# Kernel tuning notes

Hardware: AMD Instinct MI355X
Metric: run time of the kernel (lower is better)

## Reference

```python
import jax, jax.numpy as jnp
import numpy as np

GROUPS = 32
EPS = 1e-6


def _group_norm(x, scale, bias):
    B, C, H, W = x.shape
    xg = x.reshape(B, GROUPS, C // GROUPS, H, W)
    mean = xg.mean(axis=(2, 3, 4), keepdims=True)
    var = xg.var(axis=(2, 3, 4), keepdims=True)
    xg = (xg - mean) * jax.lax.rsqrt(var + EPS)
    x = xg.reshape(B, C, H, W)
    return x * scale[None, :, None, None] + bias[None, :, None, None]


def setup_inputs() -> dict:
    key = jax.random.key(0)
    ks = jax.random.split(key, 8)
    B, C, H, W = 4, 256, 64, 64
    s = 1.0 / np.sqrt(C)
    return {
        "x": jax.random.normal(ks[0], (B, C, H, W), jnp.float32),
        "gn_scale": jnp.ones((C,), jnp.float32),
        "gn_bias": jnp.zeros((C,), jnp.float32),
        "wq": jax.random.normal(ks[1], (C, C), jnp.float32) * s,
        "bq": jnp.zeros((C,), jnp.float32),
        "wk": jax.random.normal(ks[2], (C, C), jnp.float32) * s,
        "bk": jnp.zeros((C,), jnp.float32),
        "wv": jax.random.normal(ks[3], (C, C), jnp.float32) * s,
        "bv": jnp.zeros((C,), jnp.float32),
        "wp": jax.random.normal(ks[4], (C, C), jnp.float32) * s,
        "bp": jnp.zeros((C,), jnp.float32),
    }


def reference(x, gn_scale, gn_bias, wq, bq, wk, bk, wv, bv, wp, bp):
    B, C, H, W = x.shape
    hw = H * W
    o = _group_norm(x, gn_scale, gn_bias)           # [B,C,H,W]
    of = o.reshape(B, C, hw)                         # [B,C,hw]
    # 1x1 convs == per-pixel channel matmuls
    q = jnp.einsum('oc,bcn->bno', wq, of) + bq[None, None, :]   # [B,hw,C]
    k = jnp.einsum('oc,bcn->bon', wk, of) + bk[None, :, None]   # [B,C,hw]
    v = jnp.einsum('oc,bcn->bon', wv, of) + bv[None, :, None]   # [B,C,hw]
    w = jnp.einsum('bic,bcj->bij', q, k) * (C ** -0.5)          # [B,hw,hw]
    w = jax.nn.softmax(w, axis=2)
    # o[b,c,i] = sum_j v[b,c,j] * w[b,i,j]
    attn = jnp.einsum('bcj,bij->bci', v, w)          # [B,C,hw]
    # faithful to original: reshape to (B,C,W,H) (requires H==W)
    attn = attn.reshape(B, C, W, H)
    out = jnp.einsum('oc,bchw->bohw', wp, attn) + bp[None, :, None, None]
    return out + x
```

## Files before the change

### kernel.cpp

```cpp
#include <hip/hip_runtime.h>
#include <hip/hip_bf16.h>

#define NB 4
#define NC 256
#define NHW 4096
#define CPG 8
#define GEPS 1e-6f

typedef __hip_bfloat16 bf16;
typedef __attribute__((ext_vector_type(8))) short bf16x8;
typedef __attribute__((ext_vector_type(4))) float f32x4;
typedef __attribute__((ext_vector_type(8))) unsigned short u16x8;

#define MFMA16(A,B,C) __builtin_amdgcn_mfma_f32_16x16x32_bf16(A,B,C,0,0,0)

typedef __attribute__((address_space(1))) const unsigned int as1_uint;
typedef __attribute__((address_space(3))) unsigned int as3_uint;
__device__ __forceinline__ void gload_lds16(const void* g, void* l){
  __builtin_amdgcn_global_load_lds((as1_uint*)g, (as3_uint*)l, 16, 0, 0);
}

__device__ __forceinline__ float u2f(unsigned short u){
  union { unsigned u32; float f; } w; w.u32 = ((unsigned)u) << 16; return w.f;
}
__device__ __forceinline__ bf16 f2b(float v){ return __float2bfloat16(v); }
__device__ __forceinline__ unsigned short f2bu(float v){
  union { bf16 h; unsigned short u; } w; w.h = __float2bfloat16(v); return w.u;
}

__global__ __launch_bounds__(256)
void gn_stats_kernel(const float* __restrict__ x, float* __restrict__ stats){
  const int bg = blockIdx.x;
  const float* p = x + (size_t)bg * (CPG * NHW);
  float s = 0.f, s2 = 0.f;
  for(int i = threadIdx.x * 4; i < CPG * NHW; i += 1024){
    float4 v = *(const float4*)(p + i);
    s  += v.x + v.y + v.z + v.w;
    s2 += v.x*v.x + v.y*v.y + v.z*v.z + v.w*v.w;
  }
  __shared__ float red[256];
  red[threadIdx.x] = s; __syncthreads();
  for(int t = 128; t > 0; t >>= 1){
    if(threadIdx.x < t) red[threadIdx.x] += red[threadIdx.x + t];
    __syncthreads();
  }
  float sum = red[0]; __syncthreads();
  red[threadIdx.x] = s2; __syncthreads();
  for(int t = 128; t > 0; t >>= 1){
    if(threadIdx.x < t) red[threadIdx.x] += red[threadIdx.x + t];
    __syncthreads();
  }
  if(threadIdx.x == 0){
    const float inv_n = 1.f / (float)(CPG * NHW);
    float mean = sum * inv_n;
    float var = red[0] * inv_n - mean * mean;
    if(var < 0.f) var = 0.f;
    stats[bg * 2]     = mean;
    stats[bg * 2 + 1] = rsqrtf(var + GEPS);
  }
}

__global__ __launch_bounds__(256)
void wprep_kernel(const float* __restrict__ wq, const float* __restrict__ wk,
                  const float* __restrict__ wv, const float* __restrict__ wp,
                  const float* __restrict__ bq, const float* __restrict__ bk,
                  const float* __restrict__ bv,
                  bf16* __restrict__ wqkv, bf16* __restrict__ wpb, float* __restrict__ bqs){
  int i = blockIdx.x * 256 + threadIdx.x;
  if(i < 196608){
    float v;
    if(i < 65536)       v = wq[i] * 0.0625f;
    else if(i < 131072) v = wk[i - 65536];
    else                v = wv[i - 131072];
    wqkv[i] = f2b(v);
  } else {
    int j = i - 196608;
    wpb[j] = f2b(wp[j]);
  }
  if(i < 768) bqs[i] = (i < 256) ? bq[i] * 0.0625f : (i < 512 ? bk[i - 256] : bv[i - 512]);
}

__global__ __launch_bounds__(256)
void gn_prep_kernel(const float* __restrict__ x, const float* __restrict__ stats,
                    const float* __restrict__ gsc, const float* __restrict__ gbi,
                    bf16* __restrict__ xt){
  const int b = blockIdx.z, cB = blockIdx.y * 64, nB = blockIdx.x * 64;
  __shared__ unsigned short Tt[64][80];
  const int tid = threadIdx.x;
  const float* xb = x + ((size_t)(b * NC + cB)) * NHW + nB;
  #pragma unroll
  for(int pass = 0; pass < 4; pass++){
    int c_loc = (tid >> 4) + pass * 16;
    int n0 = (tid & 15) * 4;
    float4 v = *(const float4*)(xb + (size_t)c_loc * NHW + n0);
    int c_abs = cB + c_loc, bg = b * 32 + (c_abs >> 3);
    float a = stats[bg * 2 + 1] * gsc[c_abs];
    float d = gbi[c_abs] - stats[bg * 2] * a;
    Tt[n0 + 0][c_loc] = f2bu(v.x * a + d);
    Tt[n0 + 1][c_loc] = f2bu(v.y * a + d);
    Tt[n0 + 2][c_loc] = f2bu(v.z * a + d);
    Tt[n0 + 3][c_loc] = f2bu(v.w * a + d);
  }
  __syncthreads();
  int n_loc = tid >> 2, cq = (tid & 3) * 16;
  u16x8 w0 = *(const u16x8*)&Tt[n_loc][cq];
  u16x8 w1 = *(const u16x8*)&Tt[n_loc][cq + 8];
  unsigned short* dst = (unsigned short*)xt + ((size_t)(b * NHW + nB + n_loc)) * NC + cB + cq;
  *(u16x8*)dst = w0;
  *(u16x8*)(dst + 8) = w1;
}

__global__ __launch_bounds__(256, 2)
void gemm_kernel(const bf16* __restrict__ Wb, const bf16* __restrict__ Bm,
                 const float* __restrict__ bias,
                 bf16* __restrict__ qo, bf16* __restrict__ ko, bf16* __restrict__ vo,
                 float* __restrict__ fo, const float* __restrict__ xres, int epi){
  const int nB = blockIdx.x * 128;
  const int oB = blockIdx.y * 128;
  const int tid = threadIdx.x;
  const int wave = tid >> 6, lane = tid & 63;
  const int l15 = lane & 15, quad = lane >> 4;
  const int wx = wave & 1, wy = wave >> 1;

  __shared__ __align__(16) unsigned short Ast[2][512 * 8];
  __shared__ __align__(16) unsigned short Bst[2][512 * 8];
  __shared__ __align__(16) unsigned short Tt[128 * 136];

  const short* Wp = (const short*)Wb;
  const short* Bp = (const short*)Bm;

  f32x4 acc[4][4];
  #pragma unroll
  for(int mi = 0; mi < 4; mi++)
    #pragma unroll
    for(int ni = 0; ni < 4; ni++) acc[mi][ni] = (f32x4){0.f, 0.f, 0.f, 0.f};

  #pragma unroll
  for(int t = 0; t < 2; t++){
    int qn0 = (wave * 2 + t) * 64, qn = qn0 + lane;
    int o = qn >> 2, slot = qn & 3;
    gload_lds16(Wp + (size_t)(oB + o) * NC + ((slot ^ (o & 3)) * 8), &Ast[0][qn0 * 8]);
  }
  #pragma unroll
  for(int t = 0; t < 2; t++){
    int qn0 = (wave * 2 + t) * 64, qn = qn0 + lane;
    int n = qn >> 2, slot = qn & 3;
    gload_lds16(Bp + (size_t)(nB + n) * NC + ((slot ^ (n & 3)) * 8), &Bst[0][qn0 * 8]);
  }

  for(int kt = 0; kt < 8; kt++){
    __syncthreads();
    const int p = kt & 1;
    if(kt < 7){
      const int k0 = (kt + 1) * 32;
      #pragma unroll
      for(int t = 0; t < 2; t++){
        int qn0 = (wave * 2 + t) * 64, qn = qn0 + lane;
        int o = qn >> 2, slot = qn & 3;
        gload_lds16(Wp + (size_t)(oB + o) * NC + k0 + ((slot ^ (o & 3)) * 8), &Ast[p ^ 1][qn0 * 8]);
      }
      #pragma unroll
      for(int t = 0; t < 2; t++){
        int qn0 = (wave * 2 + t) * 64, qn = qn0 + lane;
        int n = qn >> 2, slot = qn & 3;
        gload_lds16(Bp + (size_t)(nB + n) * NC + k0 + ((slot ^ (n & 3)) * 8), &Bst[p ^ 1][qn0 * 8]);
      }
    }
    bf16x8 Af[4], Bf[4];
    #pragma unroll
    for(int mi = 0; mi < 4; mi++){
      int o = wx * 64 + mi * 16 + l15;
      Af[mi] = *(const bf16x8*)&Ast[p][(o * 4 + (quad ^ (o & 3))) * 8];
    }
    #pragma unroll
    for(int ni = 0; ni < 4; ni++){
      int n = wy * 64 + ni * 16 + l15;
      Bf[ni] = *(const bf16x8*)&Bst[p][(n * 4 + (quad ^ (n & 3))) * 8];
    }
    #pragma unroll
    for(int mi = 0; mi < 4; mi++)
      #pragma unroll
      for(int ni = 0; ni < 4; ni++)
        acc[mi][ni] = MFMA16(Af[mi], Bf[ni], acc[mi][ni]);
  }

  float bi[4][4];
  #pragma unroll
  for(int mi = 0; mi < 4; mi++)
    #pragma unroll
    for(int r = 0; r < 4; r++)
      bi[mi][r] = bias[oB + wx * 64 + mi * 16 + quad * 4 + r];

  if(epi == 1){
    #pragma unroll
    for(int mi = 0; mi < 4; mi++){
      #pragma unroll
      for(int ni = 0; ni < 4; ni++){
        int na = nB + wy * 64 + ni * 16 + l15;
        #pragma unroll
        for(int r = 0; r < 4; r++){
          int c = oB + wx * 64 + mi * 16 + quad * 4 + r;
          size_t idx = ((size_t)(na >> 12) * NC + c) * NHW + (na & 4095);
          fo[idx] = acc[mi][ni][r] + bi[mi][r] + xres[idx];
        }
      }
    }
  } else if(oB >= 512){
    #pragma unroll
    for(int mi = 0; mi < 4; mi++){
      #pragma unroll
      for(int ni = 0; ni < 4; ni++){
        int na = nB + wy * 64 + ni * 16 + l15;
        #pragma unroll
        for(int r = 0; r < 4; r++){
          int c = oB - 512 + wx * 64 + mi * 16 + quad * 4 + r;
          vo[((size_t)(na >> 12) * NC + c) * NHW + (na & 4095)] = f2b(acc[mi][ni][r] + bi[mi][r]);
        }
      }
    }
  } else {
    #pragma unroll
    for(int mi = 0; mi < 4; mi++){
      int ob = wx * 64 + mi * 16 + quad * 4;
      #pragma unroll
      for(int ni = 0; ni < 4; ni++){
        int nl = wy * 64 + ni * 16 + l15;
        ushort4 pk;
        pk.x = f2bu(acc[mi][ni][0] + bi[mi][0]);
        pk.y = f2bu(acc[mi][ni][1] + bi[mi][1]);
        pk.z = f2bu(acc[mi][ni][2] + bi[mi][2]);
        pk.w = f2bu(acc[mi][ni][3] + bi[mi][3]);
        *(ushort4*)&Tt[nl * 136 + ob] = pk;
      }
    }
    __syncthreads();
    bf16* dst = (oB < 256) ? qo : ko;
    const int oc0 = oB & 255;
    int row = tid >> 1, half = tid & 1;
    unsigned short* gp = (unsigned short*)dst + (size_t)(nB + row) * NC + oc0 + half * 64;
    #pragma unroll
    for(int j = 0; j < 8; j++){
      u16x8 w = *(const u16x8*)&Tt[row * 136 + half * 64 + j * 8];
      *(u16x8*)(gp + j * 8) = w;
    }
  }
}

__global__ __launch_bounds__(256, 2)
void flash_mfma4_kernel(const bf16* __restrict__ qg, const bf16* __restrict__ ktg,
                        const bf16* __restrict__ vg, bf16* __restrict__ Opart,
                        float* __restrict__ lpart){
  const int b = blockIdx.y, h = blockIdx.z;
  const int i0 = blockIdx.x * 128;
  const int tid = threadIdx.x;
  const int wave = tid >> 6, lane = tid & 63;
  const int l15 = lane & 15, quad = lane >> 4;

  __shared__ __align__(16) unsigned short Kt[2][1024 * 8];
  __shared__ __align__(16) unsigned short Vt[2][1024 * 8];
  __shared__ __align__(16) unsigned short Pt_all[4][32 * 40];
  unsigned short* Pt = Pt_all[wave];

  bf16x8 Qf[2][8];
  #pragma unroll
  for(int ist = 0; ist < 2; ist++){
    const short* qp = (const short*)qg +
        ((size_t)b * NHW + i0 + wave * 32 + ist * 16 + l15) * NC + quad * 8;
    #pragma unroll
    for(int ks = 0; ks < 8; ks++) Qf[ist][ks] = *(const bf16x8*)(qp + ks * 32);
  }

  const short* kb = (const short*)ktg + ((size_t)b * NHW + h * 1024) * NC;
  const short* vb = (const short*)vg + (size_t)b * NC * NHW + h * 1024;

  f32x4 O[2][16];
  #pragma unroll
  for(int ist = 0; ist < 2; ist++)
    #pragma unroll
    for(int ct = 0; ct < 16; ct++) O[ist][ct] = (f32x4){0.f, 0.f, 0.f, 0.f};
  float lr0 = 0.f, lr1 = 0.f;

  #pragma unroll
  for(int t = 0; t < 4; t++){
    int qn0 = (wave * 4 + t) * 64, qn = qn0 + lane;
    int j = qn >> 5, slot = qn & 31;
    gload_lds16(kb + (size_t)j * NC + ((slot ^ (j & 7)) * 8), &Kt[0][qn0 * 8]);
  }
  #pragma unroll
  for(int t = 0; t < 4; t++){
    int qn0 = (wave * 4 + t) * 64, qn = qn0 + lane;
    int c = qn >> 2, slot = qn & 3;
    gload_lds16(vb + (size_t)c * NHW + ((slot ^ (c & 3)) * 8), &Vt[0][qn0 * 8]);
  }

  for(int jt = 0; jt < 32; jt++){
    __syncthreads();
    const int p = jt & 1;
    if(jt < 31){
      const int j0n = (jt + 1) * 32;
      #pragma unroll
      for(int t = 0; t < 4; t++){
        int qn0 = (wave * 4 + t) * 64, qn = qn0 + lane;
        int j = qn >> 5, slot = qn & 31;
        gload_lds16(kb + (size_t)(j0n + j) * NC + ((slot ^ (j & 7)) * 8), &Kt[p ^ 1][qn0 * 8]);
      }
      #pragma unroll
      for(int t = 0; t < 4; t++){
        int qn0 = (wave * 4 + t) * 64, qn = qn0 + lane;
        int c = qn >> 2, slot = qn & 3;
        gload_lds16(vb + (size_t)c * NHW + j0n + ((slot ^ (c & 3)) * 8), &Vt[p ^ 1][qn0 * 8]);
      }
    }
    f32x4 S[2][2];
    #pragma unroll
    for(int st = 0; st < 2; st++){
      S[st][0] = (f32x4){0.f, 0.f, 0.f, 0.f};
      S[st][1] = (f32x4){0.f, 0.f, 0.f, 0.f};
      const int j = st * 16 + l15;
      const unsigned short* kr = &Kt[p][(size_t)j * 256];
      #pragma unroll
      for(int ks = 0; ks < 8; ks++){
        int slot = (ks * 4 + quad) ^ (j & 7);
        bf16x8 kf = *(const bf16x8*)&kr[slot * 8];
        S[st][0] = MFMA16(kf, Qf[0][ks], S[st][0]);
        S[st][1] = MFMA16(kf, Qf[1][ks], S[st][1]);
      }
    }
    #pragma unroll
    for(int ist = 0; ist < 2; ist++){
      #pragma unroll
      for(int st = 0; st < 2; st++){
        f32x4 sv = S[st][ist];
        float p0 = __expf(sv[0]), p1 = __expf(sv[1]);
        float p2 = __expf(sv[2]), p3 = __expf(sv[3]);
        if(ist == 0) lr0 += (p0 + p1) + (p2 + p3);
        else         lr1 += (p0 + p1) + (p2 + p3);
        ushort4 pk; pk.x = f2bu(p0); pk.y = f2bu(p1); pk.z = f2bu(p2); pk.w = f2bu(p3);
        *(ushort4*)&Pt[(ist * 16 + l15) * 40 + st * 16 + quad * 4] = pk;
      }
    }
    bf16x8 Pf0 = *(const bf16x8*)&Pt[(l15) * 40 + quad * 8];
    bf16x8 Pf1 = *(const bf16x8*)&Pt[(16 + l15) * 40 + quad * 8];
    #pragma unroll
    for(int ct = 0; ct < 16; ct++){
      int c = ct * 16 + l15;
      bf16x8 vf = *(const bf16x8*)&Vt[p][(c * 4 + (quad ^ (c & 3))) * 8];
      O[0][ct] = MFMA16(Pf0, vf, O[0][ct]);
      O[1][ct] = MFMA16(Pf1, vf, O[1][ct]);
    }
  }

  lr0 += __shfl_xor(lr0, 16); lr0 += __shfl_xor(lr0, 32);
  lr1 += __shfl_xor(lr1, 16); lr1 += __shfl_xor(lr1, 32);

  const size_t hb = (size_t)(h * NB + b) * NHW;
  #pragma unroll
  for(int ist = 0; ist < 2; ist++){
    #pragma unroll
    for(int r = 0; r < 4; r++){
      int i = i0 + wave * 32 + ist * 16 + quad * 4 + r;
      unsigned short* od = (unsigned short*)Opart + (hb + i) * NC + l15;
      #pragma unroll
      for(int ct = 0; ct < 16; ct++) od[ct * 16] = f2bu(O[ist][ct][r]);
    }
  }
  if(lane < 16){
    lpart[hb + i0 + wave * 32 + l15]      = lr0;
    lpart[hb + i0 + wave * 32 + 16 + l15] = lr1;
  }
}

__global__ __launch_bounds__(256)
void flash_combine4_kernel(const bf16* __restrict__ Opart, const float* __restrict__ lpart,
                           bf16* __restrict__ attn){
  int t = blockIdx.x * 256 + threadIdx.x;
  int ng = t >> 3;
  int c0 = (t & 7) * 32;
  const int HS = NB * NHW;
  float l = lpart[ng] + lpart[HS + ng] + lpart[2 * HS + ng] + lpart[3 * HS + ng];
  float inv = 1.f / l;
  const unsigned short* O0 = (const unsigned short*)Opart + (size_t)ng * NC + c0;
  unsigned short* dst = (unsigned short*)attn + (size_t)ng * NC + c0;
  #pragma unroll
  for(int u = 0; u < 32; u += 8){
    u16x8 a0 = *(const u16x8*)(O0 + u);
    u16x8 a1 = *(const u16x8*)(O0 + (size_t)HS * NC + u);
    u16x8 a2 = *(const u16x8*)(O0 + (size_t)2 * HS * NC + u);
    u16x8 a3 = *(const u16x8*)(O0 + (size_t)3 * HS * NC + u);
    u16x8 o;
    #pragma unroll
    for(int e = 0; e < 8; e++)
      o[e] = f2bu((u2f(a0[e]) + u2f(a1[e]) + u2f(a2[e]) + u2f(a3[e])) * inv);
    *(u16x8*)(dst + u) = o;
  }
}

extern "C" void kernel_launch(void* const* d_in, const int* in_sizes, int n_in,
                              void* d_out, int out_size, void* d_ws, size_t ws_size,
                              hipStream_t stream){
  (void)in_sizes; (void)n_in; (void)out_size; (void)ws_size;
  const float* x        = (const float*)d_in[0];
  const float* gn_scale = (const float*)d_in[1];
  const float* gn_bias  = (const float*)d_in[2];
  const float* wq = (const float*)d_in[3];  const float* bq = (const float*)d_in[4];
  const float* wk = (const float*)d_in[5];  const float* bk = (const float*)d_in[6];
  const float* wv = (const float*)d_in[7];  const float* bv = (const float*)d_in[8];
  const float* wp = (const float*)d_in[9];  const float* bp = (const float*)d_in[10];
  float* out = (float*)d_out;

  char* ws = (char*)d_ws;
  const size_t MB = 1048576;
  float* stats = (float*)ws;
  float* bqs   = (float*)(ws + 4096);
  bf16* wqkv   = (bf16*)(ws + 8192);
  bf16* wpb    = (bf16*)(ws + 8192 + 393216);
  bf16* xt     = (bf16*)(ws + 1 * MB);
  bf16* Opart  = xt;
  bf16* q      = (bf16*)(ws + 33 * MB);
  bf16* k      = (bf16*)(ws + 41 * MB);
  bf16* v      = (bf16*)(ws + 49 * MB);
  float* lpart = (float*)(ws + 57 * MB);
  bf16* attn   = q;

  gn_stats_kernel<<<128, 256, 0, stream>>>(x, stats);
  wprep_kernel<<<1024, 256, 0, stream>>>(wq, wk, wv, wp, bq, bk, bv, wqkv, wpb, bqs);
  gn_prep_kernel<<<dim3(64, 4, NB), 256, 0, stream>>>(x, stats, gn_scale, gn_bias, xt);

  gemm_kernel<<<dim3(128, 6), 256, 0, stream>>>(
      wqkv, xt, bqs, q, k, v, nullptr, nullptr, 0);

  flash_mfma4_kernel<<<dim3(32, NB, 4), 256, 0, stream>>>(q, k, v, Opart, lpart);
  flash_combine4_kernel<<<512, 256, 0, stream>>>(Opart, lpart, attn);

  gemm_kernel<<<dim3(128, 2), 256, 0, stream>>>(
      wpb, attn, bp, nullptr, nullptr, nullptr, out, x, 1);
}
```

Measured before the change: 224.1 us.

## Read K straight from global in flash kernel, stage output through LDS, merge prep kernels

Measured after the change: 322.3 us. 43.8% more time.

```diff
diff --git a/kernel.cpp b/kernel.cpp
--- a/kernel.cpp
+++ b/kernel.cpp
@@ -29,7 +29,27 @@
 }
 
 __global__ __launch_bounds__(256)
-void gn_stats_kernel(const float* __restrict__ x, float* __restrict__ stats){
+void gn_stats_wprep_kernel(const float* __restrict__ x, float* __restrict__ stats,
+                           const float* __restrict__ wq, const float* __restrict__ wk,
+                           const float* __restrict__ wv, const float* __restrict__ wp,
+                           const float* __restrict__ bq, const float* __restrict__ bk,
+                           const float* __restrict__ bv,
+                           bf16* __restrict__ wqkv, bf16* __restrict__ wpb,
+                           float* __restrict__ bqs){
+  if(blockIdx.x >= 128){
+    int i = (blockIdx.x - 128) * 256 + threadIdx.x;
+    if(i < 196608){
+      float v;
+      if(i < 65536)       v = wq[i] * 0.0625f;
+      else if(i < 131072) v = wk[i - 65536];
+      else                v = wv[i - 131072];
+      wqkv[i] = f2b(v);
+    } else {
+      wpb[i - 196608] = f2b(wp[i - 196608]);
+    }
+    if(i < 768) bqs[i] = (i < 256) ? bq[i] * 0.0625f : (i < 512 ? bk[i - 256] : bv[i - 512]);
+    return;
+  }
   const int bg = blockIdx.x;
   const float* p = x + (size_t)bg * (CPG * NHW);
   float s = 0.f, s2 = 0.f;
@@ -58,26 +78,6 @@
     stats[bg * 2]     = mean;
     stats[bg * 2 + 1] = rsqrtf(var + GEPS);
   }
-}
-
-__global__ __launch_bounds__(256)
-void wprep_kernel(const float* __restrict__ wq, const float* __restrict__ wk,
-                  const float* __restrict__ wv, const float* __restrict__ wp,
-                  const float* __restrict__ bq, const float* __restrict__ bk,
-                  const float* __restrict__ bv,
-                  bf16* __restrict__ wqkv, bf16* __restrict__ wpb, float* __restrict__ bqs){
-  int i = blockIdx.x * 256 + threadIdx.x;
-  if(i < 196608){
-    float v;
-    if(i < 65536)       v = wq[i] * 0.0625f;
-    else if(i < 131072) v = wk[i - 65536];
-    else                v = wv[i - 131072];
-    wqkv[i] = f2b(v);
-  } else {
-    int j = i - 196608;
-    wpb[j] = f2b(wp[j]);
-  }
-  if(i < 768) bqs[i] = (i < 256) ? bq[i] * 0.0625f : (i < 512 ? bk[i - 256] : bv[i - 512]);
 }
 
 __global__ __launch_bounds__(256)
@@ -247,7 +247,7 @@
 }
 
 __global__ __launch_bounds__(256, 2)
-void flash_mfma4_kernel(const bf16* __restrict__ qg, const bf16* __restrict__ ktg,
+void flash_mfma5_kernel(const bf16* __restrict__ qg, const bf16* __restrict__ ktg,
                         const bf16* __restrict__ vg, bf16* __restrict__ Opart,
                         float* __restrict__ lpart){
   const int b = blockIdx.y, h = blockIdx.z;
@@ -256,7 +256,6 @@
   const int wave = tid >> 6, lane = tid & 63;
   const int l15 = lane & 15, quad = lane >> 4;
 
-  __shared__ __align__(16) unsigned short Kt[2][1024 * 8];
   __shared__ __align__(16) unsigned short Vt[2][1024 * 8];
   __shared__ __align__(16) unsigned short Pt_all[4][32 * 40];
   unsigned short* Pt = Pt_all[wave];
@@ -283,14 +282,8 @@
   #pragma unroll
   for(int t = 0; t < 4; t++){
     int qn0 = (wave * 4 + t) * 64, qn = qn0 + lane;
-    int j = qn >> 5, slot = qn & 31;
-    gload_lds16(kb + (size_t)j * NC + ((slot ^ (j & 7)) * 8), &Kt[0][qn0 * 8]);
-  }
-  #pragma unroll
-  for(int t = 0; t < 4; t++){
-    int qn0 = (wave * 4 + t) * 64, qn = qn0 + lane;
-    int c = qn >> 2, slot = qn & 3;
-    gload_lds16(vb + (size_t)c * NHW + ((slot ^ (c & 3)) * 8), &Vt[0][qn0 * 8]);
+    int c = qn >> 2, slot = qn & 3, gc = slot ^ ((c >> 1) & 3);
+    gload_lds16(vb + (size_t)c * NHW + gc * 8, &Vt[0][qn0 * 8]);
   }
 
   for(int jt = 0; jt < 32; jt++){
@@ -301,27 +294,20 @@
       #pragma unroll
       for(int t = 0; t < 4; t++){
         int qn0 = (wave * 4 + t) * 64, qn = qn0 + lane;
-        int j = qn >> 5, slot = qn & 31;
-        gload_lds16(kb + (size_t)(j0n + j) * NC + ((slot ^ (j & 7)) * 8), &Kt[p ^ 1][qn0 * 8]);
-      }
-      #pragma unroll
-      for(int t = 0; t < 4; t++){
-        int qn0 = (wave * 4 + t) * 64, qn = qn0 + lane;
-        int c = qn >> 2, slot = qn & 3;
-        gload_lds16(vb + (size_t)c * NHW + j0n + ((slot ^ (c & 3)) * 8), &Vt[p ^ 1][qn0 * 8]);
-      }
-    }
+        int c = qn >> 2, slot = qn & 3, gc = slot ^ ((c >> 1) & 3);
+        gload_lds16(vb + (size_t)c * NHW + j0n + gc * 8, &Vt[p ^ 1][qn0 * 8]);
+      }
+    }
+    const int j0 = jt * 32;
     f32x4 S[2][2];
     #pragma unroll
     for(int st = 0; st < 2; st++){
       S[st][0] = (f32x4){0.f, 0.f, 0.f, 0.f};
       S[st][1] = (f32x4){0.f, 0.f, 0.f, 0.f};
-      const int j = st * 16 + l15;
-      const unsigned short* kr = &Kt[p][(size_t)j * 256];
+      const short* kp = kb + (size_t)(j0 + st * 16 + l15) * NC + quad * 8;
       #pragma unroll
       for(int ks = 0; ks < 8; ks++){
-        int slot = (ks * 4 + quad) ^ (j & 7);
-        bf16x8 kf = *(const bf16x8*)&kr[slot * 8];
+        bf16x8 kf = *(const bf16x8*)(kp + ks * 32);
         S[st][0] = MFMA16(kf, Qf[0][ks], S[st][0]);
         S[st][1] = MFMA16(kf, Qf[1][ks], S[st][1]);
       }
@@ -344,7 +330,8 @@
     #pragma unroll
     for(int ct = 0; ct < 16; ct++){
       int c = ct * 16 + l15;
-      bf16x8 vf = *(const bf16x8*)&Vt[p][(c * 4 + (quad ^ (c & 3))) * 8];
+      int slot = quad ^ ((c >> 1) & 3);
+      bf16x8 vf = *(const bf16x8*)&Vt[p][(c * 4 + slot) * 8];
       O[0][ct] = MFMA16(Pf0, vf, O[0][ct]);
       O[1][ct] = MFMA16(Pf1, vf, O[1][ct]);
     }
@@ -353,20 +340,28 @@
   lr0 += __shfl_xor(lr0, 16); lr0 += __shfl_xor(lr0, 32);
   lr1 += __shfl_xor(lr1, 16); lr1 += __shfl_xor(lr1, 32);
 
+  __syncthreads();
+  unsigned short* Vs = &Vt[0][0] + wave * 4096;
   const size_t hb = (size_t)(h * NB + b) * NHW;
   #pragma unroll
   for(int ist = 0; ist < 2; ist++){
     #pragma unroll
-    for(int r = 0; r < 4; r++){
-      int i = i0 + wave * 32 + ist * 16 + quad * 4 + r;
-      unsigned short* od = (unsigned short*)Opart + (hb + i) * NC + l15;
-      #pragma unroll
-      for(int ct = 0; ct < 16; ct++) od[ct * 16] = f2bu(O[ist][ct][r]);
-    }
-  }
-  if(lane < 16){
-    lpart[hb + i0 + wave * 32 + l15]      = lr0;
-    lpart[hb + i0 + wave * 32 + 16 + l15] = lr1;
+    for(int r = 0; r < 4; r++)
+      #pragma unroll
+      for(int ct = 0; ct < 16; ct++)
+        Vs[(quad * 4 + r) * 256 + ct * 16 + l15] = f2bu(O[ist][ct][r]);
+    int row = lane >> 2, c0 = (lane & 3) * 64;
+    unsigned short* gp = (unsigned short*)Opart +
+        (hb + i0 + wave * 32 + ist * 16 + row) * NC + c0;
+    #pragma unroll
+    for(int t = 0; t < 8; t++){
+      u16x8 w = *(const u16x8*)&Vs[row * 256 + c0 + t * 8];
+      *(u16x8*)(gp + t * 8) = w;
+    }
+  }
+  if(lane < 32){
+    float lv = (lane < 16) ? lr0 : lr1;
+    lpart[hb + i0 + wave * 32 + lane] = lv;
   }
 }
 
@@ -422,14 +417,14 @@
   float* lpart = (float*)(ws + 57 * MB);
   bf16* attn   = q;
 
-  gn_stats_kernel<<<128, 256, 0, stream>>>(x, stats);
-  wprep_kernel<<<1024, 256, 0, stream>>>(wq, wk, wv, wp, bq, bk, bv, wqkv, wpb, bqs);
+  gn_stats_wprep_kernel<<<1152, 256, 0, stream>>>(
+      x, stats, wq, wk, wv, wp, bq, bk, bv, wqkv, wpb, bqs);
   gn_prep_kernel<<<dim3(64, 4, NB), 256, 0, stream>>>(x, stats, gn_scale, gn_bias, xt);
 
   gemm_kernel<<<dim3(128, 6), 256, 0, stream>>>(
       wqkv, xt, bqs, q, k, v, nullptr, nullptr, 0);
 
-  flash_mfma4_kernel<<<dim3(32, NB, 4), 256, 0, stream>>>(q, k, v, Opart, lpart);
+  flash_mfma5_kernel<<<dim3(32, NB, 4), 256, 0, stream>>>(q, k, v, Opart, lpart);
   flash_combine4_kernel<<<512, 256, 0, stream>>>(Opart, lpart, attn);
 
   gemm_kernel<<<dim3(128, 2), 256, 0, stream>>>(
```
